# Kernel optimization log

Hardware: AMD Instinct MI355X
Metric: run time of the kernel (lower is better)

Reference implementation:

```python
import jax, jax.numpy as jnp
import numpy as np

B, L, T = 256, 50, 20          # sentences, words/sentence, chars/word
N_CHAR, E, H = 512, 128, 128   # vocab, embed dim, hidden per direction (n_out = 2H)


def setup_inputs() -> dict:
    key = jax.random.key(0)
    ks = jax.random.split(key, 6)
    x = jax.random.randint(ks[0], (B, L, T), 0, N_CHAR)  # 0 = pad char
    embed = jax.random.uniform(ks[1], (N_CHAR, E), jnp.float32, -0.15, 0.15)
    def w(k, shape, fan):
        s = np.sqrt(6.0 / fan)
        return jax.random.uniform(k, shape, jnp.float32, -s, s)
    W_ih_f = w(ks[2], (4 * H, E), H + E)
    W_hh_f = w(ks[3], (4 * H, H), 2 * H)
    W_ih_b = w(ks[4], (4 * H, E), H + E)
    W_hh_b = w(ks[5], (4 * H, H), 2 * H)
    # combined bias b_ih + b_hh; forget-gate slice initialized to 1+1=2 as in init_lstm_weight
    b = jnp.zeros((4 * H,), jnp.float32).at[H:2 * H].set(2.0)
    return dict(x=x, embed=embed, W_ih_f=W_ih_f, W_hh_f=W_hh_f, b_f=b,
                W_ih_b=W_ih_b, W_hh_b=W_hh_b, b_b=b)


def _lstm_last(x_proj, valid, W_hh, reverse):
    # x_proj: [N, T, 4H] (input projection + bias), valid: [N, T] bool.
    # Runs a masked LSTM; returns final hidden state per sequence, matching
    # pack_padded_sequence semantics (state frozen on padded steps).
    Hh = W_hh.shape[1]
    N = x_proj.shape[0]
    xs = jnp.moveaxis(x_proj, 1, 0)              # [T, N, 4H]
    vs = jnp.moveaxis(valid, 1, 0)[..., None]    # [T, N, 1]
    if reverse:
        xs, vs = xs[::-1], vs[::-1]
    def step(carry, inp):
        h, c = carry
        xt, v = inp
        g = xt + h @ W_hh.T                      # [N, 4H]
        i, f, gg, o = jnp.split(g, 4, axis=-1)   # PyTorch gate order i,f,g,o
        c_new = jax.nn.sigmoid(f) * c + jax.nn.sigmoid(i) * jnp.tanh(gg)
        h_new = jax.nn.sigmoid(o) * jnp.tanh(c_new)
        h = jnp.where(v, h_new, h)
        c = jnp.where(v, c_new, c)
        return (h, c), None
    init = (jnp.zeros((N, Hh), x_proj.dtype), jnp.zeros((N, Hh), x_proj.dtype))
    (h, _), _ = jax.lax.scan(step, init, (xs, vs))
    return h                                     # [N, H]


def reference(x, embed, W_ih_f, W_hh_f, b_f, W_ih_b, W_hh_b, b_b):
    Bb, Ll, Tt = x.shape
    xf = x.reshape(Bb * Ll, Tt)                  # [N, T]
    lens = (xf > 0).sum(axis=1)                  # word lengths (0 = pad char)
    valid = jnp.arange(Tt)[None, :] < lens[:, None]   # [N, T]
    emb = embed[xf]                              # [N, T, E]
    h_f = _lstm_last(jnp.einsum('nte,ge->ntg', emb, W_ih_f) + b_f, valid, W_hh_f, False)
    h_b = _lstm_last(jnp.einsum('nte,ge->ntg', emb, W_ih_b) + b_b, valid, W_hh_b, True)
    reprs = jnp.concatenate([h_f, h_b], axis=-1)  # [N, 2H] = cat(unbind(hidden))
    return reprs.reshape(Bb, Ll, 2 * W_hh_f.shape[1])
```

## Files before the change

### kernel.cpp

```cpp
#include <hip/hip_runtime.h>
#include <hip/hip_bf16.h>

#define NN   12800
#define TT   20
#define HID  128
#define SPB  16

typedef __attribute__((ext_vector_type(8))) short          bf16x8;
typedef __attribute__((ext_vector_type(8))) unsigned short ushort8;
typedef __attribute__((ext_vector_type(4))) float          f32x4;

#define L2E 1.4426950408889634f
#define K2  2.8853900817779268f

__device__ float g_projV[2 * 512 * 4 * 128];
__device__ __align__(16) unsigned short g_Bpk[2 * 4 * 8 * 4 * 64 * 8];

__device__ __forceinline__ unsigned short f2bf(float f) {
    union { float f; unsigned u; } a; a.f = f;
    unsigned r = a.u + 0x7FFF + ((a.u >> 16) & 1);
    return (unsigned short)(r >> 16);
}
__device__ __forceinline__ float ex2(float x) {
#if __has_builtin(__builtin_amdgcn_exp2f)
    return __builtin_amdgcn_exp2f(x);
#else
    float r; asm("v_exp_f32 %0, %1" : "=v"(r) : "v"(x)); return r;
#endif
}

__global__ __launch_bounds__(512) void prep_proj(
    const float* __restrict__ embed,
    const float* __restrict__ Wih_f, const float* __restrict__ b_f,
    const float* __restrict__ Wih_b, const float* __restrict__ b_b)
{
    const int vg = blockIdx.x;
    const int d  = blockIdx.y;
    const int g  = threadIdx.x;
    __shared__ __align__(16) float ev[4][HID];
    ev[g >> 7][g & 127] = embed[(vg * 4 + (g >> 7)) * HID + (g & 127)];
    __syncthreads();
    const float* Wi = d ? Wih_b : Wih_f;
    const float* bb = d ? b_b : b_f;
    const f32x4* Wrow = reinterpret_cast<const f32x4*>(Wi + g * HID);
    float acc[4] = {0.f, 0.f, 0.f, 0.f};
    #pragma unroll 8
    for (int k4 = 0; k4 < 32; ++k4) {
        const f32x4 wv = Wrow[k4];
        #pragma unroll
        for (int j = 0; j < 4; ++j) {
            acc[0] = fmaf(wv[j], ev[0][k4 * 4 + j], acc[0]);
            acc[1] = fmaf(wv[j], ev[1][k4 * 4 + j], acc[1]);
            acc[2] = fmaf(wv[j], ev[2][k4 * 4 + j], acc[2]);
            acc[3] = fmaf(wv[j], ev[3][k4 * 4 + j], acc[3]);
        }
    }
    const float sc = ((g >> 7) == 2) ? K2 : L2E;
    const float bv = bb[g];
    const int slot = (g & 3) * 128 + ((g >> 2) & 15) * 8 + (g >> 6);
    #pragma unroll
    for (int v = 0; v < 4; ++v)
        g_projV[(d * 512 + vg * 4 + v) * 512 + slot] = (bv + acc[v]) * sc;
}

__global__ void prep_bpack(const float* __restrict__ Whh_f, const float* __restrict__ Whh_b)
{
    const int id = blockIdx.x * 256 + threadIdx.x;
    const int lane = id & 63;
    const int kt   = (id >> 6) & 3;
    const int nt   = (id >> 8) & 7;
    const int w    = (id >> 11) & 3;
    const int d    = id >> 13;
    const int rg   = lane >> 4;
    const float* Wh = d ? Whh_b : Whh_f;
    const int gB = (nt * 16 + (lane & 15)) * 4 + w;
    const float sc = ((gB >> 7) == 2) ? K2 : L2E;
    ushort8 o;
    #pragma unroll
    for (int i = 0; i < 8; ++i) {
        const int col = (i & 1) * 64 + (kt * 4 + rg) * 4 + (i >> 1);
        o[i] = f2bf(Wh[gB * HID + col] * sc);
    }
    reinterpret_cast<ushort8*>(g_Bpk)[id] = o;
}

#define STEP(tc, QC, QN, tn, HC, HN)                                          \
{                                                                             \
    bf16x8 A[4];                                                              \
    _Pragma("unroll")                                                         \
    for (int kt = 0; kt < 4; ++kt)                                            \
        A[kt] = *reinterpret_cast<const bf16x8*>(&HC[c0 * 136 + kt * 32 + rg * 8]); \
    f32x4 acc[8];                                                             \
    _Pragma("unroll")                                                         \
    for (int r = 0; r < 4; ++r) {                                             \
        _Pragma("unroll")                                                     \
        for (int j = 0; j < 4; ++j) {                                         \
            acc[j][r]     = QC[r][0][j];                                      \
            acc[4 + j][r] = QC[r][1][j];                                      \
        }                                                                     \
    }                                                                         \
    _Pragma("unroll")                                                         \
    for (int r = 0; r < 4; ++r) {                                             \
        const int ch = chars[(rg * 4 + r) * TT + (tn)];                       \
        const f32x4* p = reinterpret_cast<const f32x4*>(                      \
            g_projV + ((dir * 512 + ch) * 4 + w) * 128 + c0 * 8);             \
        QN[r][0] = p[0];                                                      \
        QN[r][1] = p[1];                                                      \
    }                                                                         \
    _Pragma("unroll")                                                         \
    for (int kt = 0; kt < 4; ++kt) {                                          \
        _Pragma("unroll")                                                     \
        for (int nt = 0; nt < 8; ++nt)                                        \
            acc[nt] = __builtin_amdgcn_mfma_f32_16x16x32_bf16(A[kt], B[nt][kt], acc[nt], 0, 0, 0); \
    }                                                                         \
    _Pragma("unroll")                                                         \
    for (int r = 0; r < 4; ++r) {                                             \
        const bool valid = ((tc) < len4[r]);                                  \
        float hh0, hh1;                                                       \
        {                                                                     \
            const float ei = ex2(-acc[0][r]);                                 \
            const float ef = ex2(-acc[2][r]);                                 \
            const float tg = ex2(-acc[4][r]);                                 \
            const float eo = ex2(-acc[6][r]);                                 \
            const float rf = __builtin_amdgcn_rcpf(1.0f + ef);                \
            const float rr = __builtin_amdgcn_rcpf((1.0f + ei) * (1.0f + tg));\
            const float cn = fmaf(rf, cst[0][r], fmaf(-K2, tg, K2) * rr);     \
            const float ec = ex2(-cn);                                        \
            const float r2 = __builtin_amdgcn_rcpf((1.0f + eo) * (1.0f + ec));\
            const float hn = (1.0f - ec) * r2;                                \
            cst[0][r]  = valid ? cn : cst[0][r];                              \
            hreg[0][r] = valid ? hn : hreg[0][r];                             \
            hh0 = hreg[0][r];                                                 \
        }                                                                     \
        {                                                                     \
            const float ei = ex2(-acc[1][r]);                                 \
            const float ef = ex2(-acc[3][r]);                                 \
            const float tg = ex2(-acc[5][r]);                                 \
            const float eo = ex2(-acc[7][r]);                                 \
            const float rf = __builtin_amdgcn_rcpf(1.0f + ef);                \
            const float rr = __builtin_amdgcn_rcpf((1.0f + ei) * (1.0f + tg));\
            const float cn = fmaf(rf, cst[1][r], fmaf(-K2, tg, K2) * rr);     \
            const float ec = ex2(-cn);                                        \
            const float r2 = __builtin_amdgcn_rcpf((1.0f + eo) * (1.0f + ec));\
            const float hn = (1.0f - ec) * r2;                                \
            cst[1][r]  = valid ? cn : cst[1][r];                              \
            hreg[1][r] = valid ? hn : hreg[1][r];                             \
            hh1 = hreg[1][r];                                                 \
        }                                                                     \
        unsigned hw;                                                          \
        asm("v_cvt_pk_bf16_f32 %0, %1, %2" : "=v"(hw) : "v"(hh0), "v"(hh1));  \
        *reinterpret_cast<unsigned*>(&HN[(rg * 4 + r) * 136 + (c0 * 4 + w) * 2]) = hw; \
    }                                                                         \
    __syncthreads();                                                          \
}

__global__ __launch_bounds__(256, 2) void lstm_mfma(
    const int* __restrict__ x, float* __restrict__ out)
{
    __shared__ __align__(16) unsigned short h0[SPB * 136];
    __shared__ __align__(16) unsigned short h1[SPB * 136];
    __shared__ int chars[SPB * TT];
    __shared__ int len_sh[SPB];

    const int tid  = threadIdx.x;
    const int lane = tid & 63;
    const int w    = tid >> 6;
    const int c0   = lane & 15;
    const int rg   = lane >> 4;
    const int dir  = blockIdx.y;
    const int n0   = blockIdx.x * SPB;

    for (int i = tid; i < SPB * TT; i += 256) chars[i] = x[n0 * TT + i];
    for (int i = tid; i < SPB * 136; i += 256) { h0[i] = 0; h1[i] = 0; }
    __syncthreads();
    if (tid < SPB) {
        int l = 0;
        #pragma unroll
        for (int t = 0; t < TT; ++t) l += (chars[tid * TT + t] > 0) ? 1 : 0;
        len_sh[tid] = l;
    }

    bf16x8 B[8][4];
    {
        const bf16x8* Bp = reinterpret_cast<const bf16x8*>(g_Bpk);
        #pragma unroll
        for (int nt = 0; nt < 8; ++nt)
            #pragma unroll
            for (int kt = 0; kt < 4; ++kt)
                B[nt][kt] = Bp[((((dir * 4 + w) * 8 + nt) * 4 + kt) * 64) + lane];
    }
    __syncthreads();

    int len4[4];
    #pragma unroll
    for (int r = 0; r < 4; ++r) len4[r] = len_sh[rg * 4 + r];

    float cst[2][4]  = {};
    float hreg[2][4] = {};

    f32x4 qA[4][2], qB[4][2];
    {
        const int tfirst = dir ? (TT - 1) : 0;
        #pragma unroll
        for (int r = 0; r < 4; ++r) {
            const int ch = chars[(rg * 4 + r) * TT + tfirst];
            const f32x4* p = reinterpret_cast<const f32x4*>(
                g_projV + ((dir * 512 + ch) * 4 + w) * 128 + c0 * 8);
            qA[r][0] = p[0];
            qA[r][1] = p[1];
        }
    }

    for (int step = 0; step < TT; step += 2) {
        const int t0 = dir ? (TT - 1 - step) : step;
        const int t1 = dir ? (TT - 2 - step) : (step + 1);
        const int t2 = (step + 2 < TT) ? (dir ? (TT - 3 - step) : (step + 2)) : 0;
        STEP(t0, qA, qB, t1, h0, h1)
        STEP(t1, qB, qA, t2, h1, h0)
    }

    #pragma unroll
    for (int r = 0; r < 4; ++r) {
        out[(n0 + rg * 4 + r) * 256 + dir * 128 + c0 * 4 + w]      = hreg[0][r];
        out[(n0 + rg * 4 + r) * 256 + dir * 128 + 64 + c0 * 4 + w] = hreg[1][r];
    }
}

extern "C" void kernel_launch(void* const* d_in, const int* in_sizes, int n_in,
                              void* d_out, int out_size, void* d_ws, size_t ws_size,
                              hipStream_t stream)
{
    const int*   x     = (const int*)  d_in[0];
    const float* embed = (const float*)d_in[1];
    const float* Wih_f = (const float*)d_in[2];
    const float* Whh_f = (const float*)d_in[3];
    const float* b_f   = (const float*)d_in[4];
    const float* Wih_b = (const float*)d_in[5];
    const float* Whh_b = (const float*)d_in[6];
    const float* b_b   = (const float*)d_in[7];
    float* out = (float*)d_out;

    prep_proj <<<dim3(128, 2), 512, 0, stream>>>(embed, Wih_f, b_f, Wih_b, b_b);
    prep_bpack<<<64, 256, 0, stream>>>(Whh_f, Whh_b);
    lstm_mfma <<<dim3(NN / SPB, 2), 256, 0, stream>>>(x, out);
}
```

Before: 130.3 us.

## Swap MFMA operands so weights are A and hidden state is B

Puts the recurrent weights into the MFMA A operand and the hidden state into B, so each lane's accumulator holds the four gates (i,f,g,o) of one hidden unit for one sequence. Gate math therefore runs per accumulator with no cross-register shuffling. The projection table and weight packing are re-laid out to match, so the next-step input projection becomes 8 strided vector loads that go straight into the accumulators, and the h write is one 16-byte LDS store. The intent is to cut register pressure and per-step shuffle/load overhead, at the cost of the prefetch now sitting after the gate math instead of overlapping the MFMAs.

```diff
diff --git a/kernel.cpp b/kernel.cpp
--- a/kernel.cpp
+++ b/kernel.cpp
@@ -9,12 +9,13 @@
 typedef __attribute__((ext_vector_type(8))) short          bf16x8;
 typedef __attribute__((ext_vector_type(8))) unsigned short ushort8;
 typedef __attribute__((ext_vector_type(4))) float          f32x4;
+typedef __attribute__((ext_vector_type(4))) unsigned int   uint32x4;
 
 #define L2E 1.4426950408889634f
 #define K2  2.8853900817779268f
 
-__device__ float g_projV[2 * 512 * 4 * 128];
-__device__ __align__(16) unsigned short g_Bpk[2 * 4 * 8 * 4 * 64 * 8];
+__device__ float g_projV[2 * 512 * 512];
+__device__ __align__(16) unsigned short g_Apk[2 * 4 * 8 * 4 * 64 * 8];
 
 __device__ __forceinline__ unsigned short f2bf(float f) {
     union { float f; unsigned u; } a; a.f = f;
@@ -55,15 +56,16 @@
             acc[3] = fmaf(wv[j], ev[3][k4 * 4 + j], acc[3]);
         }
     }
-    const float sc = ((g >> 7) == 2) ? K2 : L2E;
+    const int q = g >> 7, u = g & 127;
+    const float sc = (q == 2) ? K2 : L2E;
     const float bv = bb[g];
-    const int slot = (g & 3) * 128 + ((g >> 2) & 15) * 8 + (g >> 6);
+    const int slot = (u & 3) * 128 + (u >> 4) * 16 + ((u >> 2) & 3) * 4 + q;
     #pragma unroll
     for (int v = 0; v < 4; ++v)
         g_projV[(d * 512 + vg * 4 + v) * 512 + slot] = (bv + acc[v]) * sc;
 }
 
-__global__ void prep_bpack(const float* __restrict__ Whh_f, const float* __restrict__ Whh_b)
+__global__ void prep_apack(const float* __restrict__ Whh_f, const float* __restrict__ Whh_b)
 {
     const int id = blockIdx.x * 256 + threadIdx.x;
     const int lane = id & 63;
@@ -71,90 +73,71 @@
     const int nt   = (id >> 8) & 7;
     const int w    = (id >> 11) & 3;
     const int d    = id >> 13;
-    const int rg   = lane >> 4;
+    const int r    = lane & 15;
+    const int rgl  = lane >> 4;
     const float* Wh = d ? Whh_b : Whh_f;
-    const int gB = (nt * 16 + (lane & 15)) * 4 + w;
-    const float sc = ((gB >> 7) == 2) ? K2 : L2E;
+    const int q    = r & 3;
+    const int unit = (nt * 4 + (r >> 2)) * 4 + w;
+    const int row  = q * 128 + unit;
+    const float sc = (q == 2) ? K2 : L2E;
     ushort8 o;
     #pragma unroll
     for (int i = 0; i < 8; ++i) {
-        const int col = (i & 1) * 64 + (kt * 4 + rg) * 4 + (i >> 1);
-        o[i] = f2bf(Wh[gB * HID + col] * sc);
-    }
-    reinterpret_cast<ushort8*>(g_Bpk)[id] = o;
-}
-
-#define STEP(tc, QC, QN, tn, HC, HN)                                          \
+        const int p = kt * 32 + rgl * 8 + i;
+        const int col = ((p & 7) * 4 + (p >> 5)) * 4 + ((p >> 3) & 3);
+        o[i] = f2bf(Wh[row * HID + col] * sc);
+    }
+    reinterpret_cast<ushort8*>(g_Apk)[id] = o;
+}
+
+#define STEP(tc, tn, HC, HN)                                                  \
 {                                                                             \
-    bf16x8 A[4];                                                              \
+    bf16x8 Bh[4];                                                             \
     _Pragma("unroll")                                                         \
     for (int kt = 0; kt < 4; ++kt)                                            \
-        A[kt] = *reinterpret_cast<const bf16x8*>(&HC[c0 * 136 + kt * 32 + rg * 8]); \
-    f32x4 acc[8];                                                             \
-    _Pragma("unroll")                                                         \
-    for (int r = 0; r < 4; ++r) {                                             \
-        _Pragma("unroll")                                                     \
-        for (int j = 0; j < 4; ++j) {                                         \
-            acc[j][r]     = QC[r][0][j];                                      \
-            acc[4 + j][r] = QC[r][1][j];                                      \
-        }                                                                     \
-    }                                                                         \
-    _Pragma("unroll")                                                         \
-    for (int r = 0; r < 4; ++r) {                                             \
-        const int ch = chars[(rg * 4 + r) * TT + (tn)];                       \
-        const f32x4* p = reinterpret_cast<const f32x4*>(                      \
-            g_projV + ((dir * 512 + ch) * 4 + w) * 128 + c0 * 8);             \
-        QN[r][0] = p[0];                                                      \
-        QN[r][1] = p[1];                                                      \
-    }                                                                         \
+        Bh[kt] = *reinterpret_cast<const bf16x8*>(&HC[c0 * 136 + kt * 32 + rg * 8]); \
     _Pragma("unroll")                                                         \
     for (int kt = 0; kt < 4; ++kt) {                                          \
         _Pragma("unroll")                                                     \
         for (int nt = 0; nt < 8; ++nt)                                        \
-            acc[nt] = __builtin_amdgcn_mfma_f32_16x16x32_bf16(A[kt], B[nt][kt], acc[nt], 0, 0, 0); \
-    }                                                                         \
+            acc[nt] = __builtin_amdgcn_mfma_f32_16x16x32_bf16(Awh[nt][kt], Bh[kt], acc[nt], 0, 0, 0); \
+    }                                                                         \
+    const bool valid = ((tc) < len_c);                                        \
     _Pragma("unroll")                                                         \
-    for (int r = 0; r < 4; ++r) {                                             \
-        const bool valid = ((tc) < len4[r]);                                  \
-        float hh0, hh1;                                                       \
-        {                                                                     \
-            const float ei = ex2(-acc[0][r]);                                 \
-            const float ef = ex2(-acc[2][r]);                                 \
-            const float tg = ex2(-acc[4][r]);                                 \
-            const float eo = ex2(-acc[6][r]);                                 \
-            const float rf = __builtin_amdgcn_rcpf(1.0f + ef);                \
-            const float rr = __builtin_amdgcn_rcpf((1.0f + ei) * (1.0f + tg));\
-            const float cn = fmaf(rf, cst[0][r], fmaf(-K2, tg, K2) * rr);     \
-            const float ec = ex2(-cn);                                        \
-            const float r2 = __builtin_amdgcn_rcpf((1.0f + eo) * (1.0f + ec));\
-            const float hn = (1.0f - ec) * r2;                                \
-            cst[0][r]  = valid ? cn : cst[0][r];                              \
-            hreg[0][r] = valid ? hn : hreg[0][r];                             \
-            hh0 = hreg[0][r];                                                 \
-        }                                                                     \
-        {                                                                     \
-            const float ei = ex2(-acc[1][r]);                                 \
-            const float ef = ex2(-acc[3][r]);                                 \
-            const float tg = ex2(-acc[5][r]);                                 \
-            const float eo = ex2(-acc[7][r]);                                 \
-            const float rf = __builtin_amdgcn_rcpf(1.0f + ef);                \
-            const float rr = __builtin_amdgcn_rcpf((1.0f + ei) * (1.0f + tg));\
-            const float cn = fmaf(rf, cst[1][r], fmaf(-K2, tg, K2) * rr);     \
-            const float ec = ex2(-cn);                                        \
-            const float r2 = __builtin_amdgcn_rcpf((1.0f + eo) * (1.0f + ec));\
-            const float hn = (1.0f - ec) * r2;                                \
-            cst[1][r]  = valid ? cn : cst[1][r];                              \
-            hreg[1][r] = valid ? hn : hreg[1][r];                             \
-            hh1 = hreg[1][r];                                                 \
-        }                                                                     \
-        unsigned hw;                                                          \
-        asm("v_cvt_pk_bf16_f32 %0, %1, %2" : "=v"(hw) : "v"(hh0), "v"(hh1));  \
-        *reinterpret_cast<unsigned*>(&HN[(rg * 4 + r) * 136 + (c0 * 4 + w) * 2]) = hw; \
+    for (int nt = 0; nt < 8; ++nt) {                                          \
+        const float ei = ex2(-acc[nt][0]);                                    \
+        const float ef = ex2(-acc[nt][1]);                                    \
+        const float tg = ex2(-acc[nt][2]);                                    \
+        const float eo = ex2(-acc[nt][3]);                                    \
+        const float rf = __builtin_amdgcn_rcpf(1.0f + ef);                    \
+        const float rr = __builtin_amdgcn_rcpf((1.0f + ei) * (1.0f + tg));    \
+        const float cn = fmaf(rf, cst[nt], fmaf(-K2, tg, K2) * rr);           \
+        const float ec = ex2(-cn);                                            \
+        const float r2 = __builtin_amdgcn_rcpf((1.0f + eo) * (1.0f + ec));    \
+        const float hn = (1.0f - ec) * r2;                                    \
+        cst[nt]  = valid ? cn : cst[nt];                                      \
+        hreg[nt] = valid ? hn : hreg[nt];                                     \
+    }                                                                         \
+    {                                                                         \
+        unsigned h0w, h1w, h2w, h3w;                                          \
+        asm("v_cvt_pk_bf16_f32 %0, %1, %2" : "=v"(h0w) : "v"(hreg[0]), "v"(hreg[1])); \
+        asm("v_cvt_pk_bf16_f32 %0, %1, %2" : "=v"(h1w) : "v"(hreg[2]), "v"(hreg[3])); \
+        asm("v_cvt_pk_bf16_f32 %0, %1, %2" : "=v"(h2w) : "v"(hreg[4]), "v"(hreg[5])); \
+        asm("v_cvt_pk_bf16_f32 %0, %1, %2" : "=v"(h3w) : "v"(hreg[6]), "v"(hreg[7])); \
+        const uint32x4 hv = {h0w, h1w, h2w, h3w};                             \
+        *reinterpret_cast<uint32x4*>(&HN[c0 * 136 + (rg * 4 + w) * 8]) = hv;  \
+    }                                                                         \
+    {                                                                         \
+        const int ch = chars[c0 * TT + (tn)];                                 \
+        const f32x4* p = reinterpret_cast<const f32x4*>(                      \
+            g_projV + (dir * 512 + ch) * 512 + w * 128 + rg * 4);             \
+        _Pragma("unroll")                                                     \
+        for (int nt = 0; nt < 8; ++nt) acc[nt] = p[nt * 4];                   \
     }                                                                         \
     __syncthreads();                                                          \
 }
 
-__global__ __launch_bounds__(256, 2) void lstm_mfma(
+__global__ __launch_bounds__(256, 2) void lstm_swp(
     const int* __restrict__ x, float* __restrict__ out)
 {
     __shared__ __align__(16) unsigned short h0[SPB * 136];
@@ -180,50 +163,42 @@
         len_sh[tid] = l;
     }
 
-    bf16x8 B[8][4];
+    bf16x8 Awh[8][4];
     {
-        const bf16x8* Bp = reinterpret_cast<const bf16x8*>(g_Bpk);
+        const bf16x8* Ap = reinterpret_cast<const bf16x8*>(g_Apk);
         #pragma unroll
         for (int nt = 0; nt < 8; ++nt)
             #pragma unroll
             for (int kt = 0; kt < 4; ++kt)
-                B[nt][kt] = Bp[((((dir * 4 + w) * 8 + nt) * 4 + kt) * 64) + lane];
-    }
-    __syncthreads();
-
-    int len4[4];
-    #pragma unroll
-    for (int r = 0; r < 4; ++r) len4[r] = len_sh[rg * 4 + r];
-
-    float cst[2][4]  = {};
-    float hreg[2][4] = {};
-
-    f32x4 qA[4][2], qB[4][2];
+                Awh[nt][kt] = Ap[((((dir * 4 + w) * 8 + nt) * 4 + kt) * 64) + lane];
+    }
+    f32x4 acc[8];
     {
         const int tfirst = dir ? (TT - 1) : 0;
-        #pragma unroll
-        for (int r = 0; r < 4; ++r) {
-            const int ch = chars[(rg * 4 + r) * TT + tfirst];
-            const f32x4* p = reinterpret_cast<const f32x4*>(
-                g_projV + ((dir * 512 + ch) * 4 + w) * 128 + c0 * 8);
-            qA[r][0] = p[0];
-            qA[r][1] = p[1];
-        }
-    }
+        const int ch = chars[c0 * TT + tfirst];
+        const f32x4* p = reinterpret_cast<const f32x4*>(
+            g_projV + (dir * 512 + ch) * 512 + w * 128 + rg * 4);
+        #pragma unroll
+        for (int nt = 0; nt < 8; ++nt) acc[nt] = p[nt * 4];
+    }
+    __syncthreads();
+
+    const int len_c = len_sh[c0];
+
+    float cst[8]  = {};
+    float hreg[8] = {};
 
     for (int step = 0; step < TT; step += 2) {
         const int t0 = dir ? (TT - 1 - step) : step;
         const int t1 = dir ? (TT - 2 - step) : (step + 1);
         const int t2 = (step + 2 < TT) ? (dir ? (TT - 3 - step) : (step + 2)) : 0;
-        STEP(t0, qA, qB, t1, h0, h1)
-        STEP(t1, qB, qA, t2, h1, h0)
+        STEP(t0, t1, h0, h1)
+        STEP(t1, t2, h1, h0)
     }
 
     #pragma unroll
-    for (int r = 0; r < 4; ++r) {
-        out[(n0 + rg * 4 + r) * 256 + dir * 128 + c0 * 4 + w]      = hreg[0][r];
-        out[(n0 + rg * 4 + r) * 256 + dir * 128 + 64 + c0 * 4 + w] = hreg[1][r];
-    }
+    for (int nt = 0; nt < 8; ++nt)
+        out[(n0 + c0) * 256 + dir * 128 + (nt * 4 + rg) * 4 + w] = hreg[nt];
 }
 
 extern "C" void kernel_launch(void* const* d_in, const int* in_sizes, int n_in,
@@ -241,6 +216,6 @@
     float* out = (float*)d_out;
 
     prep_proj <<<dim3(128, 2), 512, 0, stream>>>(embed, Wih_f, b_f, Wih_b, b_b);
-    prep_bpack<<<64, 256, 0, stream>>>(Whh_f, Whh_b);
-    lstm_mfma <<<dim3(NN / SPB, 2), 256, 0, stream>>>(x, out);
-}
+    prep_apack<<<64, 256, 0, stream>>>(Whh_f, Whh_b);
+    lstm_swp  <<<dim3(NN / SPB, 2), 256, 0, stream>>>(x, out);
+}
```

After: 167.7 us. +28.6%, slower.
